# Kernel optimization log

Measured on AMD Instinct MI355X. Metric: run time of the kernel, lower is better.

The kernel has to match this reference:

```python
import jax, jax.numpy as jnp
import numpy as np

N = 100000       # nodes
E = 3200000      # edges (avg degree 32)
F_IN = 256
F_OUT = 256
RADIUS = 3
EPS = 1e-3       # keras BatchNormalization default epsilon


def setup_inputs() -> dict:
    key = jax.random.key(0)
    ks = jax.random.split(key, 16)
    s_in = 1.0 / np.sqrt(F_IN).astype(np.float32)
    inp = {
        'x': jax.random.normal(ks[0], (N, F_IN), jnp.float32),
        'edge_row': jax.random.randint(ks[1], (E,), 0, N, jnp.int32),
        'edge_col': jax.random.randint(ks[2], (E,), 0, N, jnp.int32),
        'edge_val': jax.random.uniform(ks[3], (E,), jnp.float32),
        # stacked Dense kernels (use_bias=False): 3 applied to x, RADIUS applied to hop tensors
        'wa_x': jax.random.normal(ks[4], (3, F_IN, F_OUT), jnp.float32) * s_in,
        'wa_adj': jax.random.normal(ks[5], (RADIUS, F_IN, F_OUT), jnp.float32) * s_in,
        'wb_x': jax.random.normal(ks[6], (3, F_IN, F_OUT), jnp.float32) * s_in,
        'wb_adj': jax.random.normal(ks[7], (RADIUS, F_IN, F_OUT), jnp.float32) * s_in,
        # BatchNorm (inference-mode) params, per feature (axis=1)
        'bn_a_gamma': jax.random.uniform(ks[8], (F_OUT,), jnp.float32, 0.5, 1.5),
        'bn_a_beta': jax.random.normal(ks[9], (F_OUT,), jnp.float32) * 0.1,
        'bn_a_mean': jax.random.normal(ks[10], (F_OUT,), jnp.float32) * 0.1,
        'bn_a_var': jax.random.uniform(ks[11], (F_OUT,), jnp.float32, 0.5, 1.5),
        'bn_b_gamma': jax.random.uniform(ks[12], (F_OUT,), jnp.float32, 0.5, 1.5),
        'bn_b_beta': jax.random.normal(ks[13], (F_OUT,), jnp.float32) * 0.1,
        'bn_b_mean': jax.random.normal(ks[14], (F_OUT,), jnp.float32) * 0.1,
        'bn_b_var': jax.random.uniform(ks[15], (F_OUT,), jnp.float32, 0.5, 1.5),
    }
    return inp


def _bn(h, gamma, beta, mean, var):
    # keras BatchNormalization(axis=1), training=False: per-feature affine with moving stats
    return (h - mean) * (gamma * jax.lax.rsqrt(var + EPS)) + beta


def reference(x, edge_row, edge_col, edge_val, wa_x, wa_adj, wb_x, wb_adj,
              bn_a_gamma, bn_a_beta, bn_a_mean, bn_a_var,
              bn_b_gamma, bn_b_beta, bn_b_mean, bn_b_var):
    def spmm(h):  # y[i] = sum_j A[i,j] h[j]
        return jax.ops.segment_sum(edge_val[:, None] * h[edge_col], edge_row,
                                   num_segments=N)

    hops = [spmm(x)]
    for i in range(RADIUS - 1):
        h = hops[-1]
        for _ in range(2 ** i):
            h = spmm(h)
        hops.append(h)
    hops = jnp.stack(hops)  # [RADIUS, N, F_IN]

    # alpha1(x)+alpha2(x)+alpha3(x) == x @ (W1+W2+W3)
    alpha = x @ jnp.sum(wa_x, axis=0) + jnp.einsum('kni,kio->no', hops, wa_adj)
    alpha = _bn(jax.nn.relu(alpha), bn_a_gamma, bn_a_beta, bn_a_mean, bn_a_var)

    beta = x @ jnp.sum(wb_x, axis=0) + jnp.einsum('kni,kio->no', hops, wb_adj)
    beta = _bn(beta, bn_b_gamma, bn_b_beta, bn_b_mean, bn_b_var)

    return jnp.concatenate((alpha, beta), axis=1)  # [N, 2*F_OUT]
```

## Files before the change

### kernel.cpp

```cpp
#include <hip/hip_runtime.h>
#include <math.h>

#define N_NODES 100000
#define N_EDGES 3200000
#define F_IN 256
#define M_OUT 512
#define K_TOT 1024
#define EPS_BN 1e-3f
#define NUM_CHUNKS 391

typedef __attribute__((ext_vector_type(8))) short short8;
typedef __attribute__((ext_vector_type(4))) float floatx4;

__device__ __forceinline__ ushort f2b(float f) {
    union { float f; unsigned u; } c; c.f = f;
    unsigned u = c.u;
    unsigned r = (u + 0x7FFFu + ((u >> 16) & 1u)) >> 16;
    return (ushort)r;
}
__device__ __forceinline__ float b2f(ushort b) {
    union { unsigned u; float f; } c; c.u = ((unsigned)b) << 16;
    return c.f;
}


__global__ void zero_i32(int* __restrict__ p, int n) {
    int i = blockIdx.x * blockDim.x + threadIdx.x;
    if (i < n) p[i] = 0;
}

__global__ void hist_kernel(const int* __restrict__ row, int* __restrict__ counts, int n) {
    int i = blockIdx.x * blockDim.x + threadIdx.x;
    if (i < n) atomicAdd(&counts[row[i]], 1);
}

__global__ void scan_chunk_sums(const int* __restrict__ counts, int* __restrict__ chunkSums, int n) {
    __shared__ int sm[256];
    int c = blockIdx.x;
    int t = threadIdx.x;
    int i = c * 256 + t;
    sm[t] = (i < n) ? counts[i] : 0;
    __syncthreads();
    for (int s = 128; s > 0; s >>= 1) {
        if (t < s) sm[t] += sm[t + s];
        __syncthreads();
    }
    if (t == 0) chunkSums[c] = sm[0];
}

__global__ void scan_spine(int* __restrict__ chunkSums, int numChunks, int* __restrict__ row_off, int n) {
    __shared__ int sm[512];
    int t = threadIdx.x;
    int v = (t < numChunks) ? chunkSums[t] : 0;
    sm[t] = v;
    __syncthreads();
    for (int s = 1; s < 512; s <<= 1) {
        int add = (t >= s) ? sm[t - s] : 0;
        __syncthreads();
        sm[t] += add;
        __syncthreads();
    }
    if (t < numChunks) chunkSums[t] = sm[t] - v;
    if (t == 511) row_off[n] = sm[511];
}

__global__ void scan_final(const int* __restrict__ counts, const int* __restrict__ chunkSums,
                           int* __restrict__ row_off, int n) {
    __shared__ int sm[256];
    int c = blockIdx.x;
    int t = threadIdx.x;
    int i = c * 256 + t;
    int v = (i < n) ? counts[i] : 0;
    sm[t] = v;
    __syncthreads();
    for (int s = 1; s < 256; s <<= 1) {
        int add = (t >= s) ? sm[t - s] : 0;
        __syncthreads();
        sm[t] += add;
        __syncthreads();
    }
    if (i < n) row_off[i] = chunkSums[c] + sm[t] - v;
}

__global__ void scatter_kernel(const int* __restrict__ row, const int* __restrict__ col,
                               const float* __restrict__ val,
                               const int* __restrict__ row_off, int* __restrict__ cursor,
                               int* __restrict__ col_s, float* __restrict__ val_s, int n) {
    int i = blockIdx.x * blockDim.x + threadIdx.x;
    if (i < n) {
        int r = row[i];
        int pos = row_off[r] + atomicAdd(&cursor[r], 1);
        col_s[pos] = col[i];
        val_s[pos] = val[i];
    }
}


__global__ void convert_x(const float* __restrict__ x, ushort* __restrict__ Ab) {
    int gid = blockIdx.x * blockDim.x + threadIdx.x;
    if (gid >= N_NODES * F_IN / 4) return;
    int li = gid * 4;
    int node = li >> 8;
    int c = li & 255;
    float4 v = *reinterpret_cast<const float4*>(&x[li]);
    ushort4 o;
    o.x = f2b(v.x); o.y = f2b(v.y); o.z = f2b(v.z); o.w = f2b(v.w);
    *reinterpret_cast<ushort4*>(&Ab[(size_t)node * K_TOT + c]) = o;
}


__global__ void spmm_bf16(const int* __restrict__ row_off, const int* __restrict__ col_s,
                          const float* __restrict__ val_s,
                          const ushort* __restrict__ h, int hs,
                          ushort* __restrict__ y, int ys) {
    int wave = threadIdx.x >> 6;
    int lane = threadIdx.x & 63;
    int row = blockIdx.x * 4 + wave;
    if (row >= N_NODES) return;
    int s = row_off[row];
    int e = row_off[row + 1];
    const size_t loff = (size_t)lane * 4;

    float ax0 = 0.f, ay0 = 0.f, az0 = 0.f, aw0 = 0.f;
    float ax1 = 0.f, ay1 = 0.f, az1 = 0.f, aw1 = 0.f;

    int j = s;
    for (; j + 8 <= e; j += 8) {
        int   c[8];
        float v[8];
#pragma unroll
        for (int u = 0; u < 8; u++) { c[u] = col_s[j + u]; v[u] = val_s[j + u]; }
        ushort4 g[8];
#pragma unroll
        for (int u = 0; u < 8; u++)
            g[u] = *reinterpret_cast<const ushort4*>(&h[(size_t)c[u] * hs + loff]);
#pragma unroll
        for (int u = 0; u < 8; u += 2) {
            ax0 += v[u] * b2f(g[u].x);
            ay0 += v[u] * b2f(g[u].y);
            az0 += v[u] * b2f(g[u].z);
            aw0 += v[u] * b2f(g[u].w);
            ax1 += v[u + 1] * b2f(g[u + 1].x);
            ay1 += v[u + 1] * b2f(g[u + 1].y);
            az1 += v[u + 1] * b2f(g[u + 1].z);
            aw1 += v[u + 1] * b2f(g[u + 1].w);
        }
    }
    for (; j < e; j++) {
        int c = col_s[j];
        float v = val_s[j];
        ushort4 hv = *reinterpret_cast<const ushort4*>(&h[(size_t)c * hs + loff]);
        ax0 += v * b2f(hv.x);
        ay0 += v * b2f(hv.y);
        az0 += v * b2f(hv.z);
        aw0 += v * b2f(hv.w);
    }
    ushort4 o;
    o.x = f2b(ax0 + ax1);
    o.y = f2b(ay0 + ay1);
    o.z = f2b(az0 + az1);
    o.w = f2b(aw0 + aw1);
    *reinterpret_cast<ushort4*>(&y[(size_t)row * ys + lane * 4]) = o;
}


__global__ void build_weights_t(const float* __restrict__ wa_x, const float* __restrict__ wa_adj,
                                const float* __restrict__ wb_x, const float* __restrict__ wb_adj,
                                ushort* __restrict__ Wt) {
    int idx = blockIdx.x * blockDim.x + threadIdx.x;
    if (idx >= M_OUT * K_TOT) return;
    int n = idx >> 10;
    int kg = idx & 1023;
    int seg = kg >> 8;
    int k = kg & 255;
    float w;
    if (seg == 0) {
        if (n < 256)
            w = wa_x[0 * 65536 + k * 256 + n] + wa_x[1 * 65536 + k * 256 + n] + wa_x[2 * 65536 + k * 256 + n];
        else {
            int nn = n - 256;
            w = wb_x[0 * 65536 + k * 256 + nn] + wb_x[1 * 65536 + k * 256 + nn] + wb_x[2 * 65536 + k * 256 + nn];
        }
    } else {
        int s = seg - 1;
        if (n < 256) w = wa_adj[s * 65536 + k * 256 + n];
        else         w = wb_adj[s * 65536 + k * 256 + (n - 256)];
    }
    Wt[idx] = f2b(w);
}

__global__ void build_bn(const float* __restrict__ ga, const float* __restrict__ ba,
                         const float* __restrict__ ma, const float* __restrict__ va,
                         const float* __restrict__ gb, const float* __restrict__ bb,
                         const float* __restrict__ mb, const float* __restrict__ vb,
                         float* __restrict__ scale, float* __restrict__ bias) {
    int c = blockIdx.x * blockDim.x + threadIdx.x;
    if (c >= 512) return;
    float g, b, m, v;
    if (c < 256) { g = ga[c]; b = ba[c]; m = ma[c]; v = va[c]; }
    else { int cc = c - 256; g = gb[cc]; b = bb[cc]; m = mb[cc]; v = vb[cc]; }
    float s = g / sqrtf(v + EPS_BN);
    scale[c] = s;
    bias[c] = b - m * s;
}


#define LDS_STRIDE 40

__global__ void gemm_mfma(const ushort* __restrict__ Ab, const ushort* __restrict__ Wt,
                          float* __restrict__ C,
                          const float* __restrict__ scale, const float* __restrict__ bias) {
    __shared__ ushort As[128 * LDS_STRIDE];
    __shared__ ushort Bs[128 * LDS_STRIDE];
    const int tid = threadIdx.x;
    const int lane = tid & 63;
    const int wave = tid >> 6;
    const int wm = wave >> 1;
    const int wn = wave & 1;
    const int quad = lane >> 4;
    const int l16 = lane & 15;
    const int mBase = blockIdx.y * 128;
    const int nBase = blockIdx.x * 128;

    floatx4 acc[4][4];
#pragma unroll
    for (int i = 0; i < 4; i++)
#pragma unroll
        for (int j = 0; j < 4; j++) acc[i][j] = (floatx4){0.f, 0.f, 0.f, 0.f};

    for (int k0 = 0; k0 < K_TOT; k0 += 32) {
#pragma unroll
        for (int p = 0; p < 2; p++) {
            int li = tid + p * 256;
            int row = li >> 2;
            int c8 = (li & 3) * 8;
            int gm = mBase + row; if (gm > N_NODES - 1) gm = N_NODES - 1;
            uint4 va = *reinterpret_cast<const uint4*>(&Ab[(size_t)gm * K_TOT + k0 + c8]);
            uint4 vb = *reinterpret_cast<const uint4*>(&Wt[(size_t)(nBase + row) * K_TOT + k0 + c8]);
            *reinterpret_cast<uint4*>(&As[row * LDS_STRIDE + c8]) = va;
            *reinterpret_cast<uint4*>(&Bs[row * LDS_STRIDE + c8]) = vb;
        }
        __syncthreads();

        short8 a_frag[4], b_frag[4];
#pragma unroll
        for (int i = 0; i < 4; i++)
            a_frag[i] = *reinterpret_cast<const short8*>(&As[(wm * 64 + i * 16 + l16) * LDS_STRIDE + quad * 8]);
#pragma unroll
        for (int j = 0; j < 4; j++)
            b_frag[j] = *reinterpret_cast<const short8*>(&Bs[(wn * 64 + j * 16 + l16) * LDS_STRIDE + quad * 8]);
#pragma unroll
        for (int i = 0; i < 4; i++)
#pragma unroll
            for (int j = 0; j < 4; j++)
                acc[i][j] = __builtin_amdgcn_mfma_f32_16x16x32_bf16(a_frag[i], b_frag[j], acc[i][j], 0, 0, 0);
        __syncthreads();
    }

    float sc[4], bs[4];
    int gncol[4];
#pragma unroll
    for (int j = 0; j < 4; j++) {
        int gn = nBase + wn * 64 + j * 16 + l16;
        gncol[j] = gn;
        sc[j] = scale[gn];
        bs[j] = bias[gn];
    }
#pragma unroll
    for (int i = 0; i < 4; i++) {
#pragma unroll
        for (int r = 0; r < 4; r++) {
            int gm = mBase + wm * 64 + i * 16 + quad * 4 + r;
            if (gm >= N_NODES) continue;
#pragma unroll
            for (int j = 0; j < 4; j++) {
                float v = acc[i][j][r];
                if (gncol[j] < 256) v = fmaxf(v, 0.f);
                v = v * sc[j] + bs[j];
                C[(size_t)gm * M_OUT + gncol[j]] = v;
            }
        }
    }
}


static inline size_t align_up(size_t x, size_t a) { return (x + a - 1) & ~(a - 1); }

extern "C" void kernel_launch(void* const* d_in, const int* in_sizes, int n_in,
                              void* d_out, int out_size, void* d_ws, size_t ws_size,
                              hipStream_t stream) {
    const float* x      = (const float*)d_in[0];
    const int*   erow   = (const int*)d_in[1];
    const int*   ecol   = (const int*)d_in[2];
    const float* eval   = (const float*)d_in[3];
    const float* wa_x   = (const float*)d_in[4];
    const float* wa_adj = (const float*)d_in[5];
    const float* wb_x   = (const float*)d_in[6];
    const float* wb_adj = (const float*)d_in[7];
    const float* ga = (const float*)d_in[8];
    const float* ba = (const float*)d_in[9];
    const float* ma = (const float*)d_in[10];
    const float* va = (const float*)d_in[11];
    const float* gb = (const float*)d_in[12];
    const float* bb = (const float*)d_in[13];
    const float* mb = (const float*)d_in[14];
    const float* vb = (const float*)d_in[15];
    float* out = (float*)d_out;

    char* ws = (char*)d_ws;
    size_t off = 0;
    int*    row_off   = (int*)(ws + off);    off = align_up(off + (size_t)(N_NODES + 1) * 4, 1024);
    int*    cursor    = (int*)(ws + off);    off = align_up(off + (size_t)N_NODES * 4, 1024);
    int*    chunkSums = (int*)(ws + off);    off = align_up(off + (size_t)NUM_CHUNKS * 4, 1024);
    int*    col_s     = (int*)(ws + off);    off = align_up(off + (size_t)N_EDGES * 4, 1024);
    float*  val_s     = (float*)(ws + off);  off = align_up(off + (size_t)N_EDGES * 4, 1024);
    ushort* Wt        = (ushort*)(ws + off); off = align_up(off + (size_t)M_OUT * K_TOT * 2, 1024);
    float*  scale     = (float*)(ws + off);  off = align_up(off + 512 * 4, 1024);
    float*  bias      = (float*)(ws + off);  off = align_up(off + 512 * 4, 1024);
    ushort* Ab        = (ushort*)(ws + off); off = align_up(off + (size_t)N_NODES * K_TOT * 2, 1024);
    ushort* tmp       = (ushort*)(ws + off); off = align_up(off + (size_t)N_NODES * F_IN * 2, 1024);
    (void)ws_size; (void)in_sizes; (void)n_in; (void)out_size;

    const int zeroBlocks = (N_NODES + 255) / 256;
    const int edgeBlocks = (N_EDGES + 255) / 256;

    zero_i32<<<zeroBlocks, 256, 0, stream>>>(cursor, N_NODES);
    hist_kernel<<<edgeBlocks, 256, 0, stream>>>(erow, cursor, N_EDGES);
    scan_chunk_sums<<<NUM_CHUNKS, 256, 0, stream>>>(cursor, chunkSums, N_NODES);
    scan_spine<<<1, 512, 0, stream>>>(chunkSums, NUM_CHUNKS, row_off, N_NODES);
    scan_final<<<NUM_CHUNKS, 256, 0, stream>>>(cursor, chunkSums, row_off, N_NODES);
    zero_i32<<<zeroBlocks, 256, 0, stream>>>(cursor, N_NODES);
    scatter_kernel<<<edgeBlocks, 256, 0, stream>>>(erow, ecol, eval, row_off, cursor,
                                                   col_s, val_s, N_EDGES);

    build_weights_t<<<(M_OUT * K_TOT) / 256, 256, 0, stream>>>(wa_x, wa_adj, wb_x, wb_adj, Wt);
    build_bn<<<2, 256, 0, stream>>>(ga, ba, ma, va, gb, bb, mb, vb, scale, bias);

    convert_x<<<(N_NODES * F_IN / 4 + 255) / 256, 256, 0, stream>>>(x, Ab);

    const int spmmBlocks = (N_NODES + 3) / 4;
    spmm_bf16<<<spmmBlocks, 256, 0, stream>>>(row_off, col_s, val_s,
                                              Ab + 0 * 256, K_TOT, Ab + 1 * 256, K_TOT);
    spmm_bf16<<<spmmBlocks, 256, 0, stream>>>(row_off, col_s, val_s,
                                              Ab + 1 * 256, K_TOT, Ab + 2 * 256, K_TOT);
    spmm_bf16<<<spmmBlocks, 256, 0, stream>>>(row_off, col_s, val_s,
                                              Ab + 2 * 256, K_TOT, tmp, F_IN);
    spmm_bf16<<<spmmBlocks, 256, 0, stream>>>(row_off, col_s, val_s,
                                              tmp, F_IN, Ab + 3 * 256, K_TOT);

    dim3 gemmGrid(M_OUT / 128, (N_NODES + 127) / 128);
    gemm_mfma<<<gemmGrid, 256, 0, stream>>>(Ab, Wt, out, scale, bias);
}
```

Baseline: 1.685 ms.

## Two-pass bucketed CSR scatter and interleave column/value pairs

```diff
diff --git a/kernel.cpp b/kernel.cpp
--- a/kernel.cpp
+++ b/kernel.cpp
@@ -8,6 +8,8 @@
 #define K_TOT 1024
 #define EPS_BN 1e-3f
 #define NUM_CHUNKS 391
+#define NB NUM_CHUNKS
+#define EPB 16384
 
 typedef __attribute__((ext_vector_type(8))) short short8;
 typedef __attribute__((ext_vector_type(4))) float floatx4;
@@ -82,16 +84,60 @@
     if (i < n) row_off[i] = chunkSums[c] + sm[t] - v;
 }
 
-__global__ void scatter_kernel(const int* __restrict__ row, const int* __restrict__ col,
-                               const float* __restrict__ val,
-                               const int* __restrict__ row_off, int* __restrict__ cursor,
-                               int* __restrict__ col_s, float* __restrict__ val_s, int n) {
-    int i = blockIdx.x * blockDim.x + threadIdx.x;
-    if (i < n) {
+
+__global__ void scatter_pass1(const int* __restrict__ row, const int* __restrict__ col,
+                              const float* __restrict__ val,
+                              const int* __restrict__ bucketOff, int* __restrict__ gcur,
+                              int2* __restrict__ tmpE) {
+    __shared__ int cnt[NB];
+    __shared__ int base[NB];
+    const int t = threadIdx.x;
+    const int bs = blockIdx.x * EPB;
+    const int be = min(N_EDGES, bs + EPB);
+    for (int b = t; b < NB; b += 256) cnt[b] = 0;
+    __syncthreads();
+    for (int i = bs + t; i < be; i += 256) {
+        atomicAdd(&cnt[row[i] >> 8], 1);
+    }
+    __syncthreads();
+    for (int b = t; b < NB; b += 256) {
+        int c = cnt[b];
+        base[b] = bucketOff[b] + (c ? atomicAdd(&gcur[b], c) : 0);
+        cnt[b] = 0;
+    }
+    __syncthreads();
+    for (int i = bs + t; i < be; i += 256) {
         int r = row[i];
-        int pos = row_off[r] + atomicAdd(&cursor[r], 1);
-        col_s[pos] = col[i];
-        val_s[pos] = val[i];
+        int b = r >> 8;
+        int pos = base[b] + atomicAdd(&cnt[b], 1);
+        int2 e;
+        e.x = (col[i] << 8) | (r & 255);
+        e.y = __float_as_int(val[i]);
+        tmpE[pos] = e;
+    }
+}
+
+__global__ void scatter_pass2(const int2* __restrict__ tmpE, const int* __restrict__ bucketOff,
+                              const int* __restrict__ row_off, int2* __restrict__ csr) {
+    __shared__ int lcur[256];
+    __shared__ int roff[256];
+    const int b = blockIdx.x;
+    const int t = threadIdx.x;
+    const int rowBase = b << 8;
+    const int gr = rowBase + t;
+    lcur[t] = 0;
+    roff[t] = (gr < N_NODES) ? row_off[gr] : 0;
+    __syncthreads();
+    const int segStart = bucketOff[b];
+    const int segEnd = (b == NB - 1) ? N_EDGES : bucketOff[b + 1];
+    for (int i = segStart + t; i < segEnd; i += 256) {
+        int2 e = tmpE[i];
+        int rl = e.x & 255;
+        int pos = roff[rl] + atomicAdd(&lcur[rl], 1);
+        int2 o;
+        o.x = e.x >> 8;
+        o.y = e.y;
+        csr[pos] = o;
     }
 }
 
@@ -109,8 +155,7 @@
 }
 
 
-__global__ void spmm_bf16(const int* __restrict__ row_off, const int* __restrict__ col_s,
-                          const float* __restrict__ val_s,
+__global__ void spmm_bf16(const int* __restrict__ row_off, const int2* __restrict__ csr,
                           const ushort* __restrict__ h, int hs,
                           ushort* __restrict__ y, int ys) {
     int wave = threadIdx.x >> 6;
@@ -126,30 +171,31 @@
 
     int j = s;
     for (; j + 8 <= e; j += 8) {
-        int   c[8];
-        float v[8];
-#pragma unroll
-        for (int u = 0; u < 8; u++) { c[u] = col_s[j + u]; v[u] = val_s[j + u]; }
+        int2 ev[8];
+#pragma unroll
+        for (int u = 0; u < 8; u++) ev[u] = csr[j + u];
         ushort4 g[8];
 #pragma unroll
         for (int u = 0; u < 8; u++)
-            g[u] = *reinterpret_cast<const ushort4*>(&h[(size_t)c[u] * hs + loff]);
+            g[u] = *reinterpret_cast<const ushort4*>(&h[(size_t)ev[u].x * hs + loff]);
 #pragma unroll
         for (int u = 0; u < 8; u += 2) {
-            ax0 += v[u] * b2f(g[u].x);
-            ay0 += v[u] * b2f(g[u].y);
-            az0 += v[u] * b2f(g[u].z);
-            aw0 += v[u] * b2f(g[u].w);
-            ax1 += v[u + 1] * b2f(g[u + 1].x);
-            ay1 += v[u + 1] * b2f(g[u + 1].y);
-            az1 += v[u + 1] * b2f(g[u + 1].z);
-            aw1 += v[u + 1] * b2f(g[u + 1].w);
+            float v0 = __int_as_float(ev[u].y);
+            float v1 = __int_as_float(ev[u + 1].y);
+            ax0 += v0 * b2f(g[u].x);
+            ay0 += v0 * b2f(g[u].y);
+            az0 += v0 * b2f(g[u].z);
+            aw0 += v0 * b2f(g[u].w);
+            ax1 += v1 * b2f(g[u + 1].x);
+            ay1 += v1 * b2f(g[u + 1].y);
+            az1 += v1 * b2f(g[u + 1].z);
+            aw1 += v1 * b2f(g[u + 1].w);
         }
     }
     for (; j < e; j++) {
-        int c = col_s[j];
-        float v = val_s[j];
-        ushort4 hv = *reinterpret_cast<const ushort4*>(&h[(size_t)c * hs + loff]);
+        int2 ev = csr[j];
+        float v = __int_as_float(ev.y);
+        ushort4 hv = *reinterpret_cast<const ushort4*>(&h[(size_t)ev.x * hs + loff]);
         ax0 += v * b2f(hv.x);
         ay0 += v * b2f(hv.y);
         az0 += v * b2f(hv.z);
@@ -312,26 +358,27 @@
     int*    row_off   = (int*)(ws + off);    off = align_up(off + (size_t)(N_NODES + 1) * 4, 1024);
     int*    cursor    = (int*)(ws + off);    off = align_up(off + (size_t)N_NODES * 4, 1024);
     int*    chunkSums = (int*)(ws + off);    off = align_up(off + (size_t)NUM_CHUNKS * 4, 1024);
-    int*    col_s     = (int*)(ws + off);    off = align_up(off + (size_t)N_EDGES * 4, 1024);
-    float*  val_s     = (float*)(ws + off);  off = align_up(off + (size_t)N_EDGES * 4, 1024);
+    int2*   csr       = (int2*)(ws + off);   off = align_up(off + (size_t)N_EDGES * 8, 1024);
     ushort* Wt        = (ushort*)(ws + off); off = align_up(off + (size_t)M_OUT * K_TOT * 2, 1024);
     float*  scale     = (float*)(ws + off);  off = align_up(off + 512 * 4, 1024);
     float*  bias      = (float*)(ws + off);  off = align_up(off + 512 * 4, 1024);
     ushort* Ab        = (ushort*)(ws + off); off = align_up(off + (size_t)N_NODES * K_TOT * 2, 1024);
     ushort* tmp       = (ushort*)(ws + off); off = align_up(off + (size_t)N_NODES * F_IN * 2, 1024);
+    int2*   tmpE      = (int2*)tmp;
     (void)ws_size; (void)in_sizes; (void)n_in; (void)out_size;
 
     const int zeroBlocks = (N_NODES + 255) / 256;
     const int edgeBlocks = (N_EDGES + 255) / 256;
+    const int p1Blocks = (N_EDGES + EPB - 1) / EPB;
 
     zero_i32<<<zeroBlocks, 256, 0, stream>>>(cursor, N_NODES);
     hist_kernel<<<edgeBlocks, 256, 0, stream>>>(erow, cursor, N_EDGES);
     scan_chunk_sums<<<NUM_CHUNKS, 256, 0, stream>>>(cursor, chunkSums, N_NODES);
     scan_spine<<<1, 512, 0, stream>>>(chunkSums, NUM_CHUNKS, row_off, N_NODES);
     scan_final<<<NUM_CHUNKS, 256, 0, stream>>>(cursor, chunkSums, row_off, N_NODES);
-    zero_i32<<<zeroBlocks, 256, 0, stream>>>(cursor, N_NODES);
-    scatter_kernel<<<edgeBlocks, 256, 0, stream>>>(erow, ecol, eval, row_off, cursor,
-                                                   col_s, val_s, N_EDGES);
+    zero_i32<<<(NB + 255) / 256, 256, 0, stream>>>(cursor, NB);
+    scatter_pass1<<<p1Blocks, 256, 0, stream>>>(erow, ecol, eval, chunkSums, cursor, tmpE);
+    scatter_pass2<<<NB, 256, 0, stream>>>(tmpE, chunkSums, row_off, csr);
 
     build_weights_t<<<(M_OUT * K_TOT) / 256, 256, 0, stream>>>(wa_x, wa_adj, wb_x, wb_adj, Wt);
     build_bn<<<2, 256, 0, stream>>>(ga, ba, ma, va, gb, bb, mb, vb, scale, bias);
@@ -339,13 +386,13 @@
     convert_x<<<(N_NODES * F_IN / 4 + 255) / 256, 256, 0, stream>>>(x, Ab);
 
     const int spmmBlocks = (N_NODES + 3) / 4;
-    spmm_bf16<<<spmmBlocks, 256, 0, stream>>>(row_off, col_s, val_s,
+    spmm_bf16<<<spmmBlocks, 256, 0, stream>>>(row_off, csr,
                                               Ab + 0 * 256, K_TOT, Ab + 1 * 256, K_TOT);
-    spmm_bf16<<<spmmBlocks, 256, 0, stream>>>(row_off, col_s, val_s,
+    spmm_bf16<<<spmmBlocks, 256, 0, stream>>>(row_off, csr,
                                               Ab + 1 * 256, K_TOT, Ab + 2 * 256, K_TOT);
-    spmm_bf16<<<spmmBlocks, 256, 0, stream>>>(row_off, col_s, val_s,
+    spmm_bf16<<<spmmBlocks, 256, 0, stream>>>(row_off, csr,
                                               Ab + 2 * 256, K_TOT, tmp, F_IN);
-    spmm_bf16<<<spmmBlocks, 256, 0, stream>>>(row_off, col_s, val_s,
+    spmm_bf16<<<spmmBlocks, 256, 0, stream>>>(row_off, csr,
                                               tmp, F_IN, Ab + 3 * 256, K_TOT);
 
     dim3 gemmGrid(M_OUT / 128, (N_NODES + 127) / 128);
```

Measured after the change: 1.592 ms. -5.5%, faster.
